# Optimization experiments

Measured on AMD Instinct MI355X. Metric: run time of the kernel, lower is better.

The kernel has to match this reference:

```python
import jax, jax.numpy as jnp
import numpy as np

K = 2           # top-k experts
TEMP = 1.0      # router temperature


def setup_inputs() -> dict:
    key = jax.random.key(0)
    k0, k1, k2, k3 = jax.random.split(key, 4)
    B, T, C, E = 4, 8192, 1024, 64
    x = jax.random.normal(k0, (B, T, C), dtype=jnp.float32)
    cond = jax.random.normal(k1, (B, C), dtype=jnp.float32)
    # nn.Linear weights: gate (E, C), cond_proj (C, 2C)
    Wg = jax.random.normal(k2, (E, C), dtype=jnp.float32) * 0.02
    Wc = jax.random.normal(k3, (C, 2 * C), dtype=jnp.float32) * 0.02
    return {"x": x, "cond": cond, "Wg": Wg, "Wc": Wc}


def reference(x, cond, Wg, Wc):
    B, T, C = x.shape
    E = Wg.shape[0]
    # conditioning path: broadcast cond over tokens, concat, project
    c_exp = jnp.broadcast_to(cond[:, None, :], (B, T, C))
    hc = jnp.concatenate([x, c_exp], axis=-1)          # (B,T,2C)
    h = jnp.einsum('btd,cd->btc', hc, Wc)              # (B,T,C)
    logits = jnp.einsum('btc,ec->bte', h, Wg) * (1.0 / TEMP)  # (B,T,E)
    probs = jax.nn.softmax(logits, axis=-1)
    topk_vals, idx = jax.lax.top_k(logits, K)          # (B,T,K), sorted desc
    scores = jax.nn.softmax(topk_vals, axis=-1)
    # aux stats (no_grad in torch)
    importance = jax.lax.stop_gradient(jnp.mean(probs, axis=(0, 1)))  # (E,)
    counts = jnp.zeros((E,), probs.dtype).at[idx.reshape(-1)].add(1.0)
    load = counts / jnp.clip(jnp.sum(counts), 1.0)
    load = jax.lax.stop_gradient(load)
    return (idx, scores, probs, importance, load)
```

## Files before the change

kernel.cpp:

```cpp
#include <hip/hip_runtime.h>
#include <math.h>

#define B_    4
#define T_    8192
#define C_    1024
#define E_    64
#define NTOK  (B_*T_)
#define KSEL  2

#define OFF_IDX    0
#define OFF_SCORES (NTOK*KSEL)
#define OFF_PROBS  (2*NTOK*KSEL)
#define OFF_IMP    (OFF_PROBS + NTOK*E_)
#define OFF_LOAD   (OFF_IMP + E_)

#define WS_W32    0
#define WS_BSWH   262144
#define WS_BSWL   393216
#define WS_LB64   524288
#define WS_CNT    526336
#define WS_LIST   526400

#define REFINE_CAP 8192
#define REFINE_EPS 3e-4f

typedef __attribute__((ext_vector_type(8))) short short8;
typedef __attribute__((ext_vector_type(4))) float f32x4;

#define BAR() do { asm volatile("" ::: "memory"); \
                   __builtin_amdgcn_s_barrier();  \
                   asm volatile("" ::: "memory"); } while (0)

#define GL0(dst, p)    asm volatile("global_load_dwordx4 %0, %1, off" \
                                    : "=v"(dst) : "v"(p) : "memory")
#define GL1K(dst, p)   asm volatile("global_load_dwordx4 %0, %1, off offset:1024" \
                                    : "=v"(dst) : "v"(p) : "memory")

__global__ __launch_bounds__(256) void k_prep(const float* __restrict__ Wg,
                                              const float* __restrict__ Wc,
                                              const float* __restrict__ cond,
                                              float* __restrict__ wcomb32,
                                              short* __restrict__ bswH,
                                              short* __restrict__ bswL,
                                              double* __restrict__ lbias64,
                                              float* __restrict__ out) {
    __shared__ float wg_s[64 * 64];
    __shared__ float wc_s[64 * 4];
    __shared__ double red[256];

    const int tid = threadIdx.x;
    const int e   = tid & 63;
    const int dg  = tid >> 6;
    const int d0  = blockIdx.x * 4;

    if (blockIdx.x == 0 && tid < 2 * E_) out[OFF_IMP + tid] = 0.f;

    double ae = 0.0, ao = 0.0;

    for (int c0 = 0; c0 < C_; c0 += 64) {
        __syncthreads();
#pragma unroll
        for (int k = 0; k < 4; ++k) {
            int li = tid + k * 256;
            int r = li >> 4, c4 = (li & 15) * 4;
            float4 v = *(const float4*)&Wg[(size_t)r * 1024 + c0 + c4];
            wg_s[(c4 + 0) * 64 + r] = v.x;
            wg_s[(c4 + 1) * 64 + r] = v.y;
            wg_s[(c4 + 2) * 64 + r] = v.z;
            wg_s[(c4 + 3) * 64 + r] = v.w;
        }
        if (tid < 128) {
            int cc = tid >> 1, dd0 = (tid & 1) * 2;
            *(float2*)&wc_s[cc * 4 + dd0] =
                *(const float2*)&Wc[(size_t)(c0 + cc) * 2048 + d0 + dd0];
        }
        __syncthreads();
#pragma unroll 8
        for (int c = 0; c < 64; c += 2) {
            ae += (double)wg_s[(c + 0) * 64 + e] * (double)wc_s[(c + 0) * 4 + dg];
            ao += (double)wg_s[(c + 1) * 64 + e] * (double)wc_s[(c + 1) * 4 + dg];
        }
    }
    const double acc = ae + ao;

    if (d0 < 1024) {
        const int d = d0 + dg;
        const int et = e >> 4, nn = e & 15;
        float f = (float)acc;
        wcomb32[d * 64 + e] = f;
        unsigned u = __float_as_uint(f);
        short hi = (short)(u >> 16);
        float r = f - __uint_as_float(u & 0xFFFF0000u);
        short lo = (short)(__float_as_uint(r) >> 16);
        int kchunk = d >> 5, qsel = (d >> 3) & 3, j = d & 7;
        int idx = ((kchunk * 4 + et) * 64 + qsel * 16 + nn) * 8 + j;
        bswH[idx] = hi;
        bswL[idx] = lo;
    } else {
        const int da = d0 - 1024 + dg;
#pragma unroll
        for (int b = 0; b < 4; ++b) {
            double pb = (double)cond[b * 1024 + da] * acc;
            __syncthreads();
            red[tid] = pb;
            __syncthreads();
            if (tid < 64) {
                double s = red[tid] + red[tid + 64] + red[tid + 128] + red[tid + 192];
#if __has_builtin(__builtin_amdgcn_global_atomic_fadd_f64)
                unsafeAtomicAdd(&lbias64[b * 64 + tid], s);
#else
                atomicAdd(&lbias64[b * 64 + tid], s);
#endif
            }
        }
    }
}

__device__ __forceinline__ void split8(const float* xv, short8& h, short8& l) {
#pragma unroll
    for (int j = 0; j < 8; ++j) {
        unsigned u = __float_as_uint(xv[j]);
        h[j] = (short)(u >> 16);
        float r = xv[j] - __uint_as_float(u & 0xFFFF0000u);
        l[j] = (short)(__float_as_uint(r) >> 16);
    }
}

#define MT    32
#define ROWP  65

__device__ __forceinline__ void stage_tile(const float* __restrict__ x,
                                           float* xs, int token0, int t,
                                           int buf, int wid, int lane) {
#pragma unroll
    for (int p = 0; p < 4; ++p) {
        const int sbase = p * 256 + wid * 64;
        const int s  = sbase + lane;
        const int r  = s >> 5;
        const int f  = (s & 31) ^ (r & 7);
        const float* g = &x[(size_t)(token0 + r) * 1024 + t * 128 + f * 4];
        float* l = xs + buf * 4096 + sbase * 4;
        __builtin_amdgcn_global_load_lds(
            (const __attribute__((address_space(1))) unsigned int*)g,
            (__attribute__((address_space(3))) unsigned int*)l, 16, 0, 0);
    }
}

__global__ __launch_bounds__(256, 4) void k_main(const float* __restrict__ x,
                                                 const short* __restrict__ bswH,
                                                 const short* __restrict__ bswL,
                                                 const double* __restrict__ lbias64,
                                                 float* __restrict__ out,
                                                 unsigned int* __restrict__ ref_cnt,
                                                 int* __restrict__ ref_list) {
    __shared__ __align__(16) float xs[2 * 4096];
    __shared__ float invs[MT];
    __shared__ unsigned int cnts[E_];

    const int tid    = threadIdx.x;
    const int wid    = tid >> 6;
    const int lane   = tid & 63;
    const int nn     = lane & 15;
    const int qsel   = lane >> 4;
    const int th     = wid & 1;
    const int eh     = wid >> 1;
    const int et0    = eh * 2;
    const int token0 = blockIdx.x * MT;
    const int b      = token0 >> 13;

    if (tid < E_) cnts[tid] = 0;

    f32x4 acc[2];
#pragma unroll
    for (int ei = 0; ei < 2; ++ei) acc[ei] = (f32x4){0.f, 0.f, 0.f, 0.f};

    const char* bh0 = (const char*)(bswH + (size_t)et0 * 512 + lane * 8);
    const char* bl0 = (const char*)(bswL + (size_t)et0 * 512 + lane * 8);

    const int rr = th * 16 + nn;
    const int rx = rr & 7;

    stage_tile(x, xs, token0, 0, 0, wid, lane);

    for (int t = 0; t < 8; ++t) {
        const int cur = t & 1;

        short8 Bh[4][2], Bl[4][2];
        {
            const char* bhT = bh0 + (size_t)t * 16384;
            const char* blT = bl0 + (size_t)t * 16384;
#pragma unroll
            for (int kc = 0; kc < 4; ++kc) {
                const char* ph = bhT + kc * 4096;
                const char* pl = blT + kc * 4096;
                GL0 (Bh[kc][0], ph);
                GL1K(Bh[kc][1], ph);
                GL0 (Bl[kc][0], pl);
                GL1K(Bl[kc][1], pl);
            }
        }
        if (t < 7) stage_tile(x, xs, token0, t + 1, cur ^ 1, wid, lane);
        if (t < 7) asm volatile("s_waitcnt vmcnt(4)" ::: "memory");
        else       asm volatile("s_waitcnt vmcnt(0)" ::: "memory");
        __builtin_amdgcn_sched_barrier(0);
        BAR();

        const float* abase = xs + cur * 4096 + rr * 128;
#pragma unroll
        for (int kc = 0; kc < 4; ++kc) {
            const int f0 = kc * 8 + qsel * 2;
            float xv[8];
            *(f32x4*)&xv[0] = *(const f32x4*)(abase + (((f0    ) ^ rx) << 2));
            *(f32x4*)&xv[4] = *(const f32x4*)(abase + (((f0 + 1) ^ rx) << 2));
            short8 ah, al;
            split8(xv, ah, al);
#pragma unroll
            for (int ei = 0; ei < 2; ++ei) {
                acc[ei] = __builtin_amdgcn_mfma_f32_16x16x32_bf16(ah, Bh[kc][ei], acc[ei], 0, 0, 0);
                acc[ei] = __builtin_amdgcn_mfma_f32_16x16x32_bf16(ah, Bl[kc][ei], acc[ei], 0, 0, 0);
                acc[ei] = __builtin_amdgcn_mfma_f32_16x16x32_bf16(al, Bh[kc][ei], acc[ei], 0, 0, 0);
            }
        }
        BAR();
    }

    const int q4 = qsel * 4;
#pragma unroll
    for (int ei = 0; ei < 2; ++ei) {
        const int et = et0 + ei;
        float lb = (float)lbias64[b * 64 + et * 16 + nn];
#pragma unroll
        for (int r = 0; r < 4; ++r) {
            int tok = th * 16 + q4 + r;
            xs[tok * ROWP + et * 16 + nn] = acc[ei][r] + lb;
        }
    }
    __syncthreads();

    if (tid < MT) {
        const int tk = tid;
        const int base = tk * ROWP;
        float v1 = -1e30f, v2 = -1e30f, v3 = -1e30f;
        int i1 = 0, i2 = 0;
        for (int e = 0; e < E_; ++e) {
            float l = xs[base + e];
            if (l > v1)      { v3 = v2; v2 = v1; i2 = i1; v1 = l; i1 = e; }
            else if (l > v2) { v3 = v2; v2 = l; i2 = e; }
            else if (l > v3) { v3 = l; }
        }
        float sum = 0.f;
        for (int e = 0; e < E_; ++e) {
            float ex = __expf(xs[base + e] - v1);
            xs[base + e] = ex;
            sum += ex;
        }
        invs[tk] = 1.0f / sum;

        const int gt = token0 + tk;
        float s1 = 1.0f / (1.0f + __expf(v2 - v1));
        *(float2*)&out[OFF_IDX + (size_t)gt * 2]    = make_float2((float)i1, (float)i2);
        *(float2*)&out[OFF_SCORES + (size_t)gt * 2] = make_float2(s1, 1.0f - s1);
        atomicAdd(&cnts[i1], 1u);
        atomicAdd(&cnts[i2], 1u);

        float g12 = v1 - v2, g23 = v2 - v3;
        float g = g12 < g23 ? g12 : g23;
        if (g < REFINE_EPS) {
            unsigned int pos = atomicAdd(ref_cnt, 1u);
            if (pos < REFINE_CAP) ref_list[pos] = gt;
        }
    }
    __syncthreads();

    float* probs = out + OFF_PROBS + (size_t)token0 * E_;
#pragma unroll
    for (int k = 0; k < 2; ++k) {
        int li4 = tid + k * 256;
        int tok = li4 >> 4;
        int c4 = (li4 & 15) << 2;
        float inv = invs[tok];
        int o = tok * ROWP + c4;
        *(float4*)&probs[(size_t)li4 * 4] =
            make_float4(xs[o] * inv, xs[o + 1] * inv,
                        xs[o + 2] * inv, xs[o + 3] * inv);
    }

    if (tid < E_) {
        const int e = tid;
        float s = 0.f;
        for (int tt = 0; tt < MT; ++tt) s += xs[tt * ROWP + e] * invs[tt];
        atomicAdd(&out[OFF_IMP + e],  s * (1.0f / (float)NTOK));
        atomicAdd(&out[OFF_LOAD + e], (float)cnts[e] * (1.0f / (float)(NTOK * KSEL)));
    }
}

__global__ __launch_bounds__(256) void k_refine(const float* __restrict__ x,
                                                const float* __restrict__ wcomb32,
                                                const double* __restrict__ lbias64,
                                                const unsigned int* __restrict__ ref_cnt,
                                                const int* __restrict__ ref_list,
                                                float* __restrict__ out) {
    int wave = (int)((blockIdx.x * blockDim.x + threadIdx.x) >> 6);
    int lane = threadIdx.x & 63;
    unsigned int n = *ref_cnt;
    if (n > REFINE_CAP) n = REFINE_CAP;
    const int nwaves = (int)((gridDim.x * blockDim.x) >> 6);

    for (unsigned int wi = wave; wi < n; wi += nwaves) {
        const int gt = ref_list[wi];
        const int b = gt / T_;
        const float* xrow = x + (size_t)gt * C_;
        double a0 = 0.0, a1 = 0.0, a2 = 0.0, a3 = 0.0;
        for (int d = 0; d < C_; d += 4) {
            a0 += (double)xrow[d + 0] * (double)wcomb32[(d + 0) * 64 + lane];
            a1 += (double)xrow[d + 1] * (double)wcomb32[(d + 1) * 64 + lane];
            a2 += (double)xrow[d + 2] * (double)wcomb32[(d + 2) * 64 + lane];
            a3 += (double)xrow[d + 3] * (double)wcomb32[(d + 3) * 64 + lane];
        }
        double acc = ((a0 + a1) + (a2 + a3)) + lbias64[b * 64 + lane];

        double v = acc; int id = lane;
        for (int off = 32; off > 0; off >>= 1) {
            double ov = __shfl_xor(v, off, 64);
            int oid   = __shfl_xor(id, off, 64);
            if (ov > v || (ov == v && oid < id)) { v = ov; id = oid; }
        }
        double v1 = v; int i1 = id;
        v = (lane == i1) ? -1e300 : acc; id = lane;
        for (int off = 32; off > 0; off >>= 1) {
            double ov = __shfl_xor(v, off, 64);
            int oid   = __shfl_xor(id, off, 64);
            if (ov > v || (ov == v && oid < id)) { v = ov; id = oid; }
        }
        double v2 = v; int i2 = id;

        if (lane == 0) {
            float s1 = (float)(1.0 / (1.0 + exp(v2 - v1)));
            *(float2*)&out[OFF_IDX + (size_t)gt * 2]    = make_float2((float)i1, (float)i2);
            *(float2*)&out[OFF_SCORES + (size_t)gt * 2] = make_float2(s1, 1.0f - s1);
        }
    }
}

extern "C" void kernel_launch(void* const* d_in, const int* in_sizes, int n_in,
                              void* d_out, int out_size, void* d_ws, size_t ws_size,
                              hipStream_t stream) {
    const float* x    = (const float*)d_in[0];
    const float* cond = (const float*)d_in[1];
    const float* Wg   = (const float*)d_in[2];
    const float* Wc   = (const float*)d_in[3];
    float* out = (float*)d_out;
    char*  ws  = (char*)d_ws;

    float*  wcomb32 = (float*)(ws + WS_W32);
    short*  bswH    = (short*)(ws + WS_BSWH);
    short*  bswL    = (short*)(ws + WS_BSWL);
    double* lbias64 = (double*)(ws + WS_LB64);
    unsigned int* ref_cnt = (unsigned int*)(ws + WS_CNT);
    int*    ref_list = (int*)(ws + WS_LIST);

    hipMemsetAsync(ws + WS_LB64, 0, (WS_CNT - WS_LB64) + 64, stream);

    k_prep<<<512, 256, 0, stream>>>(Wg, Wc, cond, wcomb32, bswH, bswL, lbias64, out);
    k_main<<<NTOK / MT, 256, 0, stream>>>(x, bswH, bswL, lbias64, out, ref_cnt, ref_list);
    k_refine<<<256, 256, 0, stream>>>(x, wcomb32, lbias64, ref_cnt, ref_list, out);
}
```

Measured before the change: 324.2 us.

## Split B-operand loads into halves and prefetch next tile's first half

The per-tile weight-fragment loads are split into two halves held in separate register sets. The first half for the next k-tile is prefetched while the second half of the current tile computes, and the vmcnt waits are adjusted so MFMA work overlaps global load latency. Launch bounds drop from 4 to 3 waves per SIMD to make room for the extra registers, which trades occupancy for deeper software pipelining.

```diff
diff --git a/kernel.cpp b/kernel.cpp
--- a/kernel.cpp
+++ b/kernel.cpp
@@ -35,6 +35,15 @@
                                     : "=v"(dst) : "v"(p) : "memory")
 #define GL1K(dst, p)   asm volatile("global_load_dwordx4 %0, %1, off offset:1024" \
                                     : "=v"(dst) : "v"(p) : "memory")
+
+#define LOAD_BHALF(Bh_, Bl_, tt, kcbase) do {                                \
+    const char* ph_ = bh0 + (size_t)(tt) * 16384 + (kcbase) * 4096;          \
+    const char* pl_ = bl0 + (size_t)(tt) * 16384 + (kcbase) * 4096;          \
+    GL0 (Bh_[0][0], ph_);        GL1K(Bh_[0][1], ph_);                       \
+    GL0 (Bl_[0][0], pl_);        GL1K(Bl_[0][1], pl_);                       \
+    GL0 (Bh_[1][0], ph_ + 4096); GL1K(Bh_[1][1], ph_ + 4096);                \
+    GL0 (Bl_[1][0], pl_ + 4096); GL1K(Bl_[1][1], pl_ + 4096);                \
+} while (0)
 
 __global__ __launch_bounds__(256) void k_prep(const float* __restrict__ Wg,
                                               const float* __restrict__ Wc,
@@ -146,7 +155,28 @@
     }
 }
 
-__global__ __launch_bounds__(256, 4) void k_main(const float* __restrict__ x,
+__device__ __forceinline__ void compute_half(const float* abase, int kc0,
+                                             int qsel, int rx,
+                                             short8 (&Bh_)[2][2], short8 (&Bl_)[2][2],
+                                             f32x4 (&acc)[2]) {
+#pragma unroll
+    for (int k2 = 0; k2 < 2; ++k2) {
+        const int f0 = (kc0 + k2) * 8 + qsel * 2;
+        float xv[8];
+        *(f32x4*)&xv[0] = *(const f32x4*)(abase + (((f0    ) ^ rx) << 2));
+        *(f32x4*)&xv[4] = *(const f32x4*)(abase + (((f0 + 1) ^ rx) << 2));
+        short8 ah, al;
+        split8(xv, ah, al);
+#pragma unroll
+        for (int ei = 0; ei < 2; ++ei) {
+            acc[ei] = __builtin_amdgcn_mfma_f32_16x16x32_bf16(ah, Bh_[k2][ei], acc[ei], 0, 0, 0);
+            acc[ei] = __builtin_amdgcn_mfma_f32_16x16x32_bf16(ah, Bl_[k2][ei], acc[ei], 0, 0, 0);
+            acc[ei] = __builtin_amdgcn_mfma_f32_16x16x32_bf16(al, Bh_[k2][ei], acc[ei], 0, 0, 0);
+        }
+    }
+}
+
+__global__ __launch_bounds__(256, 3) void k_main(const float* __restrict__ x,
                                                  const short* __restrict__ bswH,
                                                  const short* __restrict__ bswL,
                                                  const double* __restrict__ lbias64,
@@ -180,47 +210,33 @@
     const int rr = th * 16 + nn;
     const int rx = rr & 7;
 
+    short8 BhA[2][2], BlA[2][2], BhB[2][2], BlB[2][2];
+
     stage_tile(x, xs, token0, 0, 0, wid, lane);
+    LOAD_BHALF(BhA, BlA, 0, 0);
 
     for (int t = 0; t < 8; ++t) {
         const int cur = t & 1;
 
-        short8 Bh[4][2], Bl[4][2];
-        {
-            const char* bhT = bh0 + (size_t)t * 16384;
-            const char* blT = bl0 + (size_t)t * 16384;
-#pragma unroll
-            for (int kc = 0; kc < 4; ++kc) {
-                const char* ph = bhT + kc * 4096;
-                const char* pl = blT + kc * 4096;
-                GL0 (Bh[kc][0], ph);
-                GL1K(Bh[kc][1], ph);
-                GL0 (Bl[kc][0], pl);
-                GL1K(Bl[kc][1], pl);
-            }
-        }
+        LOAD_BHALF(BhB, BlB, t, 2);
         if (t < 7) stage_tile(x, xs, token0, t + 1, cur ^ 1, wid, lane);
-        if (t < 7) asm volatile("s_waitcnt vmcnt(4)" ::: "memory");
-        else       asm volatile("s_waitcnt vmcnt(0)" ::: "memory");
+
+        if (t < 7) asm volatile("s_waitcnt vmcnt(12)" ::: "memory");
+        else       asm volatile("s_waitcnt vmcnt(8)"  ::: "memory");
         __builtin_amdgcn_sched_barrier(0);
         BAR();
 
         const float* abase = xs + cur * 4096 + rr * 128;
-#pragma unroll
-        for (int kc = 0; kc < 4; ++kc) {
-            const int f0 = kc * 8 + qsel * 2;
-            float xv[8];
-            *(f32x4*)&xv[0] = *(const f32x4*)(abase + (((f0    ) ^ rx) << 2));
-            *(f32x4*)&xv[4] = *(const f32x4*)(abase + (((f0 + 1) ^ rx) << 2));
-            short8 ah, al;
-            split8(xv, ah, al);
-#pragma unroll
-            for (int ei = 0; ei < 2; ++ei) {
-                acc[ei] = __builtin_amdgcn_mfma_f32_16x16x32_bf16(ah, Bh[kc][ei], acc[ei], 0, 0, 0);
-                acc[ei] = __builtin_amdgcn_mfma_f32_16x16x32_bf16(ah, Bl[kc][ei], acc[ei], 0, 0, 0);
-                acc[ei] = __builtin_amdgcn_mfma_f32_16x16x32_bf16(al, Bh[kc][ei], acc[ei], 0, 0, 0);
-            }
-        }
+        compute_half(abase, 0, qsel, rx, BhA, BlA, acc);
+
+        if (t < 7) LOAD_BHALF(BhA, BlA, t + 1, 0);
+
+        if (t < 7) asm volatile("s_waitcnt vmcnt(12)" ::: "memory");
+        else       asm volatile("s_waitcnt vmcnt(0)"  ::: "memory");
+        __builtin_amdgcn_sched_barrier(0);
+
+        compute_half(abase, 2, qsel, rx, BhB, BlB, acc);
+
         BAR();
     }
 
```

New measurement: 322.4 us. Within noise of the previous version (-0.5%).

## Double token tile to 64 and give each wave one expert group across all tokens

Applied to the files above, without the earlier changes.

Grows the per-block token tile from 32 to 64 and remaps the waves. Each wave now owns one 16-expert slice for all four 16-token groups, instead of a 2x2 split of tokens and experts. This cuts per-block loads of the split bf16 weight fragments relative to tokens processed, and halves the block count. The cost is doubled LDS staging (64KB), launch bounds lowered to 2 blocks per CU, and each wave splitting four A fragments per k-chunk, which duplicates fp32-to-bf16 split work across the waves.

```diff
diff --git a/kernel.cpp b/kernel.cpp
--- a/kernel.cpp
+++ b/kernel.cpp
@@ -32,8 +32,6 @@
                    asm volatile("" ::: "memory"); } while (0)
 
 #define GL0(dst, p)    asm volatile("global_load_dwordx4 %0, %1, off" \
-                                    : "=v"(dst) : "v"(p) : "memory")
-#define GL1K(dst, p)   asm volatile("global_load_dwordx4 %0, %1, off offset:1024" \
                                     : "=v"(dst) : "v"(p) : "memory")
 
 __global__ __launch_bounds__(256) void k_prep(const float* __restrict__ Wg,
@@ -126,34 +124,34 @@
     }
 }
 
-#define MT    32
+#define MT    64
 #define ROWP  65
 
 __device__ __forceinline__ void stage_tile(const float* __restrict__ x,
                                            float* xs, int token0, int t,
                                            int buf, int wid, int lane) {
 #pragma unroll
-    for (int p = 0; p < 4; ++p) {
+    for (int p = 0; p < 8; ++p) {
         const int sbase = p * 256 + wid * 64;
         const int s  = sbase + lane;
         const int r  = s >> 5;
         const int f  = (s & 31) ^ (r & 7);
         const float* g = &x[(size_t)(token0 + r) * 1024 + t * 128 + f * 4];
-        float* l = xs + buf * 4096 + sbase * 4;
+        float* l = xs + buf * 8192 + sbase * 4;
         __builtin_amdgcn_global_load_lds(
             (const __attribute__((address_space(1))) unsigned int*)g,
             (__attribute__((address_space(3))) unsigned int*)l, 16, 0, 0);
     }
 }
 
-__global__ __launch_bounds__(256, 4) void k_main(const float* __restrict__ x,
+__global__ __launch_bounds__(256, 2) void k_main(const float* __restrict__ x,
                                                  const short* __restrict__ bswH,
                                                  const short* __restrict__ bswL,
                                                  const double* __restrict__ lbias64,
                                                  float* __restrict__ out,
                                                  unsigned int* __restrict__ ref_cnt,
                                                  int* __restrict__ ref_list) {
-    __shared__ __align__(16) float xs[2 * 4096];
+    __shared__ __align__(16) float xs[2 * 8192];
     __shared__ float invs[MT];
     __shared__ unsigned int cnts[E_];
 
@@ -162,77 +160,73 @@
     const int lane   = tid & 63;
     const int nn     = lane & 15;
     const int qsel   = lane >> 4;
-    const int th     = wid & 1;
-    const int eh     = wid >> 1;
-    const int et0    = eh * 2;
     const int token0 = blockIdx.x * MT;
     const int b      = token0 >> 13;
 
     if (tid < E_) cnts[tid] = 0;
 
-    f32x4 acc[2];
-#pragma unroll
-    for (int ei = 0; ei < 2; ++ei) acc[ei] = (f32x4){0.f, 0.f, 0.f, 0.f};
-
-    const char* bh0 = (const char*)(bswH + (size_t)et0 * 512 + lane * 8);
-    const char* bl0 = (const char*)(bswL + (size_t)et0 * 512 + lane * 8);
-
-    const int rr = th * 16 + nn;
-    const int rx = rr & 7;
+    f32x4 acc[4];
+#pragma unroll
+    for (int g = 0; g < 4; ++g) acc[g] = (f32x4){0.f, 0.f, 0.f, 0.f};
+
+    const char* bh0 = (const char*)bswH + (size_t)wid * 1024 + lane * 16;
+    const char* bl0 = (const char*)bswL + (size_t)wid * 1024 + lane * 16;
 
     stage_tile(x, xs, token0, 0, 0, wid, lane);
 
     for (int t = 0; t < 8; ++t) {
         const int cur = t & 1;
 
-        short8 Bh[4][2], Bl[4][2];
+        short8 Bh[4], Bl[4];
         {
-            const char* bhT = bh0 + (size_t)t * 16384;
-            const char* blT = bl0 + (size_t)t * 16384;
+            const char* ph = bh0 + (size_t)t * 16384;
+            const char* pl = bl0 + (size_t)t * 16384;
 #pragma unroll
             for (int kc = 0; kc < 4; ++kc) {
-                const char* ph = bhT + kc * 4096;
-                const char* pl = blT + kc * 4096;
-                GL0 (Bh[kc][0], ph);
-                GL1K(Bh[kc][1], ph);
-                GL0 (Bl[kc][0], pl);
-                GL1K(Bl[kc][1], pl);
+                GL0(Bh[kc], ph + kc * 4096);
+                GL0(Bl[kc], pl + kc * 4096);
             }
         }
         if (t < 7) stage_tile(x, xs, token0, t + 1, cur ^ 1, wid, lane);
-        if (t < 7) asm volatile("s_waitcnt vmcnt(4)" ::: "memory");
+        if (t < 7) asm volatile("s_waitcnt vmcnt(8)" ::: "memory");
         else       asm volatile("s_waitcnt vmcnt(0)" ::: "memory");
         __builtin_amdgcn_sched_barrier(0);
         BAR();
 
-        const float* abase = xs + cur * 4096 + rr * 128;
+        const float* abase = xs + cur * 8192;
 #pragma unroll
         for (int kc = 0; kc < 4; ++kc) {
             const int f0 = kc * 8 + qsel * 2;
-            float xv[8];
-            *(f32x4*)&xv[0] = *(const f32x4*)(abase + (((f0    ) ^ rx) << 2));
-            *(f32x4*)&xv[4] = *(const f32x4*)(abase + (((f0 + 1) ^ rx) << 2));
-            short8 ah, al;
-            split8(xv, ah, al);
-#pragma unroll
-            for (int ei = 0; ei < 2; ++ei) {
-                acc[ei] = __builtin_amdgcn_mfma_f32_16x16x32_bf16(ah, Bh[kc][ei], acc[ei], 0, 0, 0);
-                acc[ei] = __builtin_amdgcn_mfma_f32_16x16x32_bf16(ah, Bl[kc][ei], acc[ei], 0, 0, 0);
-                acc[ei] = __builtin_amdgcn_mfma_f32_16x16x32_bf16(al, Bh[kc][ei], acc[ei], 0, 0, 0);
+            short8 ah[4], al[4];
+#pragma unroll
+            for (int g = 0; g < 4; ++g) {
+                const int rr = g * 16 + nn;
+                const int rx = rr & 7;
+                float xv[8];
+                *(f32x4*)&xv[0] = *(const f32x4*)(abase + rr * 128 + (((f0    ) ^ rx) << 2));
+                *(f32x4*)&xv[4] = *(const f32x4*)(abase + rr * 128 + (((f0 + 1) ^ rx) << 2));
+                split8(xv, ah[g], al[g]);
+            }
+#pragma unroll
+            for (int g = 0; g < 4; ++g) {
+                acc[g] = __builtin_amdgcn_mfma_f32_16x16x32_bf16(ah[g], Bh[kc], acc[g], 0, 0, 0);
+                acc[g] = __builtin_amdgcn_mfma_f32_16x16x32_bf16(ah[g], Bl[kc], acc[g], 0, 0, 0);
+                acc[g] = __builtin_amdgcn_mfma_f32_16x16x32_bf16(al[g], Bh[kc], acc[g], 0, 0, 0);
             }
         }
         BAR();
     }
 
     const int q4 = qsel * 4;
-#pragma unroll
-    for (int ei = 0; ei < 2; ++ei) {
-        const int et = et0 + ei;
-        float lb = (float)lbias64[b * 64 + et * 16 + nn];
-#pragma unroll
-        for (int r = 0; r < 4; ++r) {
-            int tok = th * 16 + q4 + r;
-            xs[tok * ROWP + et * 16 + nn] = acc[ei][r] + lb;
+    {
+        float lb = (float)lbias64[b * 64 + wid * 16 + nn];
+#pragma unroll
+        for (int g = 0; g < 4; ++g) {
+#pragma unroll
+            for (int r = 0; r < 4; ++r) {
+                int tok = g * 16 + q4 + r;
+                xs[tok * ROWP + wid * 16 + nn] = acc[g][r] + lb;
+            }
         }
     }
     __syncthreads();
@@ -274,7 +268,7 @@
 
     float* probs = out + OFF_PROBS + (size_t)token0 * E_;
 #pragma unroll
-    for (int k = 0; k < 2; ++k) {
+    for (int k = 0; k < 4; ++k) {
         int li4 = tid + k * 256;
         int tok = li4 >> 4;
         int c4 = (li4 & 15) << 2;
```

After: 325.7 us. About the same (+0.5%).
